# Kernel tuning notes

Measured on AMD Instinct MI355X. Metric: run time of the kernel, lower is better.

## Reference

```python
import jax, jax.numpy as jnp
import numpy as np

B, T, C = 2, 4096, 512
H = 8
D = C // H  # head_dim = 64


def setup_inputs() -> dict:
    key = jax.random.key(0)
    ks = jax.random.split(key, 9)
    s = 0.02
    return {
        "x": jax.random.normal(ks[0], (B, T, C), dtype=jnp.float32),
        "wq": jax.random.normal(ks[1], (C, C), dtype=jnp.float32) * s,
        "bq": jnp.zeros((C,), dtype=jnp.float32),
        "wk": jax.random.normal(ks[2], (C, C), dtype=jnp.float32) * s,
        "bk": jnp.zeros((C,), dtype=jnp.float32),
        "wv": jax.random.normal(ks[3], (C, C), dtype=jnp.float32) * s,
        "bv": jnp.zeros((C,), dtype=jnp.float32),
        "wo": jax.random.normal(ks[4], (C, C), dtype=jnp.float32) * s,
        "bo": jnp.zeros((C,), dtype=jnp.float32),
    }


def reference(x, wq, bq, wk, bk, wv, bv, wo, bo):
    Bx, Tx, Cx = x.shape
    # projections: y = x @ W^T + b (torch Linear convention: W is [out, in])
    q = (x @ wq.T + bq).reshape(Bx, Tx, H, D).transpose(0, 2, 1, 3)  # [B,H,T,D]
    k = (x @ wk.T + bk).reshape(Bx, Tx, H, D).transpose(0, 2, 1, 3)
    v = (x @ wv.T + bv).reshape(Bx, Tx, H, D).transpose(0, 2, 1, 3)
    scores = jnp.einsum("bhqd,bhkd->bhqk", q, k) * (D ** -0.5)  # [B,H,T,T]
    causal = jnp.tril(jnp.ones((Tx, Tx), dtype=bool))
    scores = jnp.where(causal, scores, -jnp.inf)
    weights = jax.nn.softmax(scores, axis=-1)
    o = jnp.einsum("bhqk,bhkd->bhqd", weights, v)  # [B,H,T,D]
    o = o.transpose(0, 2, 1, 3).reshape(Bx, Tx, Cx)
    return o @ wo.T + bo
```

## Files before the change

### kernel.cpp

```cpp
#include <hip/hip_runtime.h>
#include <math.h>

static constexpr int Bb = 2;
static constexpr int Tt = 4096;
static constexpr int Cc = 512;
static constexpr int Hh = 8;
static constexpr int Dd = 64;
static constexpr int Mtot = Bb * Tt;

#define QSCALE 0.1803368801111f
#define NTICK 1024

typedef __attribute__((ext_vector_type(8)))  short   short8;
typedef __attribute__((ext_vector_type(4)))  float   f32x4;
typedef __attribute__((ext_vector_type(16))) float   f32x16;
typedef __attribute__((ext_vector_type(4)))  unsigned int   uint4v;
typedef __attribute__((ext_vector_type(4)))  unsigned short ushort4v;

__device__ inline unsigned short f2bf(float f) {
    unsigned int u = __float_as_uint(f);
    u += 0x7fffu + ((u >> 16) & 1u);
    return (unsigned short)(u >> 16);
}
__device__ inline float bf2f(unsigned short u) {
    return __uint_as_float((unsigned int)u << 16);
}

__device__ inline unsigned int cvtpk_bf16(float a, float b) {
    unsigned int r;
    asm("v_cvt_pk_bf16_f32 %0, %1, %2" : "=v"(r) : "v"(a), "v"(b));
    return r;
}

__device__ inline int SW(int row) { return (row ^ (row >> 3)) & 7; }

__device__ inline void gload16(const void* g, void* lds) {
    __builtin_amdgcn_global_load_lds(
        (const __attribute__((address_space(1))) void*)g,
        (__attribute__((address_space(3))) void*)lds, 16, 0, 0);
}

__global__ __launch_bounds__(256)
void cast_f32_bf16(const float* __restrict__ src, unsigned short* __restrict__ dst,
                   int* __restrict__ ctr) {
    if (blockIdx.x == 0 && threadIdx.x == 0) *ctr = 0;
    const size_t i = ((size_t)blockIdx.x * 256 + threadIdx.x) * 8;
    const float4 a = *reinterpret_cast<const float4*>(src + i);
    const float4 b = *reinterpret_cast<const float4*>(src + i + 4);
    short8 o;
    o[0] = (short)f2bf(a.x); o[1] = (short)f2bf(a.y);
    o[2] = (short)f2bf(a.z); o[3] = (short)f2bf(a.w);
    o[4] = (short)f2bf(b.x); o[5] = (short)f2bf(b.y);
    o[6] = (short)f2bf(b.z); o[7] = (short)f2bf(b.w);
    *reinterpret_cast<short8*>(dst + i) = o;
}

__global__ __launch_bounds__(256)
void cast_w4(const float* __restrict__ w0, const float* __restrict__ w1,
             const float* __restrict__ w2, const float* __restrict__ w3,
             unsigned short* __restrict__ dst) {
    const float* srcs[4] = {w0, w1, w2, w3};
    const float* s = srcs[blockIdx.y];
    unsigned short* d = dst + (size_t)blockIdx.y * (Cc * Cc);
    const size_t i = ((size_t)blockIdx.x * 256 + threadIdx.x) * 8;
    const float4 a = *reinterpret_cast<const float4*>(s + i);
    const float4 b = *reinterpret_cast<const float4*>(s + i + 4);
    short8 o;
    o[0] = (short)f2bf(a.x); o[1] = (short)f2bf(a.y);
    o[2] = (short)f2bf(a.z); o[3] = (short)f2bf(a.w);
    o[4] = (short)f2bf(b.x); o[5] = (short)f2bf(b.y);
    o[6] = (short)f2bf(b.z); o[7] = (short)f2bf(b.w);
    *reinterpret_cast<short8*>(d + i) = o;
}

__global__ __launch_bounds__(256)
void proj_qkv(const unsigned short* __restrict__ A, const unsigned short* __restrict__ Wall,
              const float* __restrict__ bq, const float* __restrict__ bk,
              const float* __restrict__ bv,
              unsigned short* __restrict__ qo, unsigned short* __restrict__ ko,
              unsigned short* __restrict__ vo) {
    __shared__ unsigned short As[128][32];
    __shared__ unsigned short Bs[128][32];

    const int which = blockIdx.z;
    const unsigned short* Wb = Wall + (size_t)which * Cc * Cc;
    const float* bias = (which == 0) ? bq : (which == 1) ? bk : bv;
    unsigned short* outp = (which == 0) ? qo : (which == 1) ? ko : vo;
    const float scale = (which == 0) ? QSCALE : 1.0f;

    const int tid = threadIdx.x;
    const int lane = tid & 63;
    const int w = tid >> 6;
    const int wr = w >> 1, wc = w & 1;
    const int l15 = lane & 15, lg = lane >> 4;
    const int m0 = blockIdx.x * 128, n0 = blockIdx.y * 128;

    f32x4 acc[4][4] = {};

    for (int k0 = 0; k0 < Cc; k0 += 32) {
        #pragma unroll
        for (int i = 0; i < 2; ++i) {
            const int idx = tid + i * 256;
            const int row = idx >> 2, g = idx & 3;
            *reinterpret_cast<short8*>(&As[row][g * 8]) =
                *reinterpret_cast<const short8*>(&A[(size_t)(m0 + row) * Cc + k0 + g * 8]);
            *reinterpret_cast<short8*>(&Bs[row][g * 8]) =
                *reinterpret_cast<const short8*>(&Wb[(size_t)(n0 + row) * Cc + k0 + g * 8]);
        }
        __syncthreads();
        short8 a[4], b[4];
        #pragma unroll
        for (int mi = 0; mi < 4; ++mi)
            a[mi] = *reinterpret_cast<const short8*>(&As[wr * 64 + mi * 16 + l15][lg * 8]);
        #pragma unroll
        for (int nj = 0; nj < 4; ++nj)
            b[nj] = *reinterpret_cast<const short8*>(&Bs[wc * 64 + nj * 16 + l15][lg * 8]);
        #pragma unroll
        for (int mi = 0; mi < 4; ++mi)
            #pragma unroll
            for (int nj = 0; nj < 4; ++nj)
                acc[mi][nj] = __builtin_amdgcn_mfma_f32_16x16x32_bf16(a[mi], b[nj], acc[mi][nj], 0, 0, 0);
        __syncthreads();
    }

    #pragma unroll
    for (int mi = 0; mi < 4; ++mi) {
        #pragma unroll
        for (int nj = 0; nj < 4; ++nj) {
            const int col = n0 + wc * 64 + nj * 16 + l15;
            const float bvv = bias[col];
            if (which == 2) {
                const int mbase = m0 + wr * 64 + mi * 16 + lg * 4;
                const int b_ = mbase >> 12, t = mbase & (Tt - 1);
                const int h = col >> 6, d = col & 63;
                ushort4v o;
                #pragma unroll
                for (int r = 0; r < 4; ++r)
                    o[r] = f2bf(acc[mi][nj][r] + bvv);
                *reinterpret_cast<ushort4v*>(
                    &outp[(((size_t)b_ * Hh + h) * Dd + d) * Tt + t]) = o;
            } else {
                #pragma unroll
                for (int r = 0; r < 4; ++r) {
                    const int row = m0 + wr * 64 + mi * 16 + lg * 4 + r;
                    const int b_ = row >> 12, t = row & (Tt - 1);
                    const int h = col >> 6, d = col & 63;
                    outp[(((size_t)b_ * Hh + h) * Tt + t) * Dd + d] =
                        f2bf((acc[mi][nj][r] + bvv) * scale);
                }
            }
        }
    }
}

__global__ __launch_bounds__(256)
void proj_out(const unsigned short* __restrict__ A, const unsigned short* __restrict__ Wb,
              const float* __restrict__ bias, float* __restrict__ outp) {
    __shared__ unsigned short As[128][32];
    __shared__ unsigned short Bs[128][32];

    const int tid = threadIdx.x;
    const int lane = tid & 63;
    const int w = tid >> 6;
    const int wr = w >> 1, wc = w & 1;
    const int l15 = lane & 15, lg = lane >> 4;
    const int m0 = blockIdx.x * 128, n0 = blockIdx.y * 128;

    f32x4 acc[4][4] = {};

    for (int k0 = 0; k0 < Cc; k0 += 32) {
        #pragma unroll
        for (int i = 0; i < 2; ++i) {
            const int idx = tid + i * 256;
            const int row = idx >> 2, g = idx & 3;
            *reinterpret_cast<short8*>(&As[row][g * 8]) =
                *reinterpret_cast<const short8*>(&A[(size_t)(m0 + row) * Cc + k0 + g * 8]);
            *reinterpret_cast<short8*>(&Bs[row][g * 8]) =
                *reinterpret_cast<const short8*>(&Wb[(size_t)(n0 + row) * Cc + k0 + g * 8]);
        }
        __syncthreads();
        short8 a[4], b[4];
        #pragma unroll
        for (int mi = 0; mi < 4; ++mi)
            a[mi] = *reinterpret_cast<const short8*>(&As[wr * 64 + mi * 16 + l15][lg * 8]);
        #pragma unroll
        for (int nj = 0; nj < 4; ++nj)
            b[nj] = *reinterpret_cast<const short8*>(&Bs[wc * 64 + nj * 16 + l15][lg * 8]);
        #pragma unroll
        for (int mi = 0; mi < 4; ++mi)
            #pragma unroll
            for (int nj = 0; nj < 4; ++nj)
                acc[mi][nj] = __builtin_amdgcn_mfma_f32_16x16x32_bf16(a[mi], b[nj], acc[mi][nj], 0, 0, 0);
        __syncthreads();
    }

    #pragma unroll
    for (int mi = 0; mi < 4; ++mi) {
        #pragma unroll
        for (int nj = 0; nj < 4; ++nj) {
            const int col = n0 + wc * 64 + nj * 16 + l15;
            const float bv = bias[col];
            #pragma unroll
            for (int r = 0; r < 4; ++r) {
                const int row = m0 + wr * 64 + mi * 16 + lg * 4 + r;
                outp[(size_t)row * Cc + col] = acc[mi][nj][r] + bv;
            }
        }
    }
}

__global__ __launch_bounds__(512)
void attn_mfma(const unsigned short* __restrict__ qb, const unsigned short* __restrict__ kb,
               const unsigned short* __restrict__ vtb,
               unsigned short* __restrict__ opart, float* __restrict__ lp,
               int* __restrict__ ctr) {
    __shared__ unsigned short Ks[3][64][64];
    __shared__ unsigned short Vts[3][64][64];
    __shared__ int tkt;

    const int tid = threadIdx.x;
    const int w = tid >> 6;
    const int lane = tid & 63;
    const int l31 = lane & 31, hi = lane >> 5;

    const int r0 = (w << 3) + (lane >> 3);
    const int gk0 = ((lane & 7) ^ SW(r0)) * 8;

    for (;;) {
        __syncthreads();
        if (tid == 0) tkt = atomicAdd(ctr, 1);
        __syncthreads();
        const int t = tkt;
        if (t >= NTICK) break;

        const int qt = 15 - (t >> 6);
        const int ch = (t >> 4) & 3;
        const int bh = t & 15;
        const int t0 = (qt + 1) * ch;
        const int t1 = (qt + 1) * (ch + 1);

        const int qg = qt * 256 + w * 32 + l31;

        short8 qf[4];
        {
            const unsigned short* qp = qb + ((size_t)bh * Tt + qg) * Dd + hi * 8;
            #pragma unroll
            for (int sl = 0; sl < 4; ++sl)
                qf[sl] = *reinterpret_cast<const short8*>(qp + sl * 16);
        }

        const unsigned short* kb_h = kb + (size_t)bh * Tt * Dd;
        const unsigned short* vt_h = vtb + (size_t)bh * Dd * Tt;

        auto STAGE = [&](int kt_, int slot) {
            const int n64 = kt_ * 64;
            gload16(kb_h + (size_t)(n64 + r0) * Dd + gk0, &Ks[slot][(w << 3)][0]);
            gload16(vt_h + (size_t)r0 * Tt + n64 + gk0, &Vts[slot][(w << 3)][0]);
        };

        f32x16 oacc[2] = {};
        float lrow = 0.f;

        const int qmax_w = qt * 256 + w * 32 + 31;
        const int qmin_w = qt * 256 + w * 32;

        STAGE(t0, 0);
        if (t0 + 1 < t1) STAGE(t0 + 1, 1);

        int cur = 0;
        for (int kt = t0; kt < t1; ++kt) {
            if (kt + 1 < t1) {
                asm volatile("s_waitcnt vmcnt(2)" ::: "memory");
            } else {
                asm volatile("s_waitcnt vmcnt(0)" ::: "memory");
            }
            __builtin_amdgcn_s_barrier();
            __builtin_amdgcn_sched_barrier(0);

            if (kt + 2 < t1) {
                const int stg = (cur + 2 >= 3) ? (cur - 1) : (cur + 2);
                STAGE(kt + 2, stg);
            }

            if (kt * 64 <= qmax_w) {
                f32x16 sacc[2];
                __builtin_amdgcn_s_setprio(1);
                #pragma unroll
                for (int f = 0; f < 2; ++f) {
                    f32x16 z = {};
                    const int krow = f * 32 + l31;
                    const int sw = SW(krow);
                    #pragma unroll
                    for (int sl = 0; sl < 4; ++sl) {
                        const short8 kf = *reinterpret_cast<const short8*>(
                            &Ks[cur][krow][((2 * sl + hi) ^ sw) * 8]);
                        z = __builtin_amdgcn_mfma_f32_32x32x16_bf16(kf, qf[sl], z, 0, 0, 0);
                    }
                    sacc[f] = z;
                }
                __builtin_amdgcn_s_setprio(0);

                if (kt * 64 + 63 > qmin_w) {
                    #pragma unroll
                    for (int f = 0; f < 2; ++f)
                        #pragma unroll
                        for (int r = 0; r < 16; ++r) {
                            const int kvg = kt * 64 + f * 32 + (r & 3) + 8 * (r >> 2) + 4 * hi;
                            if (kvg > qg) sacc[f][r] = -INFINITY;
                        }
                }

                #pragma unroll
                for (int f = 0; f < 2; ++f)
                    #pragma unroll
                    for (int r = 0; r < 16; ++r)
                        sacc[f][r] = exp2f(sacc[f][r]);

                float t16[16];
                #pragma unroll
                for (int r = 0; r < 16; ++r) t16[r] = sacc[0][r] + sacc[1][r];
                #pragma unroll
                for (int r = 0; r < 8; ++r) t16[r] += t16[r + 8];
                #pragma unroll
                for (int r = 0; r < 4; ++r) t16[r] += t16[r + 4];
                t16[0] += t16[2];
                t16[1] += t16[3];
                lrow += t16[0] + t16[1];

                #pragma unroll
                for (int f = 0; f < 2; ++f) {
                    #pragma unroll
                    for (int s2 = 0; s2 < 2; ++s2) {
                        const int b0 = s2 * 8;
                        unsigned int c01 = cvtpk_bf16(sacc[f][b0 + 0], sacc[f][b0 + 1]);
                        unsigned int c23 = cvtpk_bf16(sacc[f][b0 + 2], sacc[f][b0 + 3]);
                        unsigned int c45 = cvtpk_bf16(sacc[f][b0 + 4], sacc[f][b0 + 5]);
                        unsigned int c67 = cvtpk_bf16(sacc[f][b0 + 6], sacc[f][b0 + 7]);
                        asm("v_permlane32_swap_b32 %0, %1" : "+v"(c01), "+v"(c45));
                        asm("v_permlane32_swap_b32 %0, %1" : "+v"(c23), "+v"(c67));
                        uint4v paw;
                        paw[0] = c01; paw[1] = c23; paw[2] = c45; paw[3] = c67;
                        const short8 pa = *reinterpret_cast<short8*>(&paw);
                        const int g = 4 * f + 2 * s2;
                        __builtin_amdgcn_s_setprio(1);
                        #pragma unroll
                        for (int nb = 0; nb < 2; ++nb) {
                            const int vrow = nb * 32 + l31;
                            const short8 vf = *reinterpret_cast<const short8*>(
                                &Vts[cur][vrow][((g + hi) ^ SW(vrow)) * 8]);
                            oacc[nb] = __builtin_amdgcn_mfma_f32_32x32x16_bf16(pa, vf, oacc[nb], 0, 0, 0);
                        }
                        __builtin_amdgcn_s_setprio(0);
                    }
                }
            }

            cur = (cur == 2) ? 0 : cur + 1;
        }

        const float lf = lrow + __shfl_xor(lrow, 32);
        const size_t pbase = ((size_t)ch * 16 + bh) * Tt;
        if (hi == 0) lp[pbase + qg] = lf;
        #pragma unroll
        for (int r = 0; r < 16; ++r) {
            const int qr = (r & 3) + 8 * (r >> 2) + 4 * hi;
            const int tg = qt * 256 + w * 32 + qr;
            unsigned short* dst = opart + (pbase + tg) * 64 + l31;
            dst[0]  = f2bf(oacc[0][r]);
            dst[32] = f2bf(oacc[1][r]);
        }
    }
}

__global__ __launch_bounds__(256)
void combine(const unsigned short* __restrict__ opart, const float* __restrict__ lp,
             unsigned short* __restrict__ ob) {
    const int tid = threadIdx.x;
    const int row = (int)blockIdx.x * 16 + (tid >> 4);
    const int c4 = (tid & 15) * 4;
    const size_t cs = (size_t)16 * Tt;

    const float inv = 1.f / (lp[row] + lp[cs + row] + lp[2 * cs + row] + lp[3 * cs + row]);

    const ushort4v p0 = *reinterpret_cast<const ushort4v*>(&opart[(0 * cs + row) * 64 + c4]);
    const ushort4v p1 = *reinterpret_cast<const ushort4v*>(&opart[(1 * cs + row) * 64 + c4]);
    const ushort4v p2 = *reinterpret_cast<const ushort4v*>(&opart[(2 * cs + row) * 64 + c4]);
    const ushort4v p3 = *reinterpret_cast<const ushort4v*>(&opart[(3 * cs + row) * 64 + c4]);

    ushort4v o;
    #pragma unroll
    for (int e = 0; e < 4; ++e)
        o[e] = f2bf((bf2f(p0[e]) + bf2f(p1[e]) + bf2f(p2[e]) + bf2f(p3[e])) * inv);

    const int bh = row >> 12, t = row & (Tt - 1);
    const int b_ = bh >> 3, h = bh & 7;
    *reinterpret_cast<ushort4v*>(&ob[((size_t)b_ * Tt + t) * Cc + h * Dd + c4]) = o;
}

extern "C" void kernel_launch(void* const* d_in, const int* in_sizes, int n_in,
                              void* d_out, int out_size, void* d_ws, size_t ws_size,
                              hipStream_t stream) {
    const float* x  = (const float*)d_in[0];
    const float* wq = (const float*)d_in[1];
    const float* bq = (const float*)d_in[2];
    const float* wk = (const float*)d_in[3];
    const float* bk = (const float*)d_in[4];
    const float* wv = (const float*)d_in[5];
    const float* bv = (const float*)d_in[6];
    const float* wo = (const float*)d_in[7];
    const float* bo = (const float*)d_in[8];
    float* out = (float*)d_out;

    const size_t nTok = (size_t)Mtot * Cc;
    const size_t nW   = (size_t)Cc * Cc;

    unsigned short* xb    = (unsigned short*)d_ws;
    unsigned short* wqb   = xb + nTok;
    unsigned short* wob   = wqb + 3 * nW;
    unsigned short* qbuf  = wqb + 4 * nW;
    unsigned short* kbuf  = qbuf + nTok;
    unsigned short* vtbuf = kbuf + nTok;
    unsigned short* oattb = vtbuf + nTok;
    unsigned short* opart = oattb + nTok;
    float* lp  = (float*)(opart + (size_t)4 * 16 * Tt * 64);
    int*   ctr = (int*)(lp + (size_t)4 * 16 * Tt);

    cast_f32_bf16<<<dim3((unsigned)(nTok / 8 / 256)), 256, 0, stream>>>(x, xb, ctr);
    cast_w4<<<dim3((unsigned)(nW / 8 / 256), 4), 256, 0, stream>>>(wq, wk, wv, wo, wqb);

    proj_qkv<<<dim3(Mtot / 128, Cc / 128, 3), 256, 0, stream>>>(
        xb, wqb, bq, bk, bv, qbuf, kbuf, vtbuf);

    attn_mfma<<<dim3(512), 512, 0, stream>>>(qbuf, kbuf, vtbuf, opart, lp, ctr);

    combine<<<dim3(16 * Tt / 16), 256, 0, stream>>>(opart, lp, oattb);

    proj_out<<<dim3(Mtot / 128, Cc / 128), 256, 0, stream>>>(oattb, wob, bo, out);
}
```

Before: 148.5 us.

## Fuse split-KV combine into output projection and merge cast kernels

The separate combine kernel is removed, and the output projection now reads the four bf16 partial attention outputs and row sums directly. It normalizes them while staging the A tile into XOR-swizzled LDS. The output GEMM tile shrinks to 64x128, the weight tile is loaded with global_load_lds, and the x and weight cast kernels are merged into a single launch. This saves two launches and the round trip of the combined attention output through memory. In exchange, each projection block redoes the combine work for every N tile, reading opart four times overall and adding more global loads to the GEMM loop.

```diff
diff --git a/kernel.cpp b/kernel.cpp
--- a/kernel.cpp
+++ b/kernel.cpp
@@ -41,10 +41,26 @@
 }
 
 __global__ __launch_bounds__(256)
-void cast_f32_bf16(const float* __restrict__ src, unsigned short* __restrict__ dst,
-                   int* __restrict__ ctr) {
-    if (blockIdx.x == 0 && threadIdx.x == 0) *ctr = 0;
-    const size_t i = ((size_t)blockIdx.x * 256 + threadIdx.x) * 8;
+void cast_all(const float* __restrict__ x,
+              const float* __restrict__ w0, const float* __restrict__ w1,
+              const float* __restrict__ w2, const float* __restrict__ w3,
+              unsigned short* __restrict__ xb, unsigned short* __restrict__ wb,
+              int* __restrict__ ctr) {
+    const int bid = (int)blockIdx.x;
+    if (bid == 0 && threadIdx.x == 0) *ctr = 0;
+    const float* src;
+    unsigned short* dst;
+    size_t i;
+    if (bid < 2048) {
+        src = x; dst = xb;
+        i = ((size_t)bid * 256 + threadIdx.x) * 8;
+    } else {
+        const float* srcs[4] = {w0, w1, w2, w3};
+        const int wi = (bid - 2048) >> 7;
+        src = srcs[wi];
+        dst = wb + (size_t)wi * (Cc * Cc);
+        i = ((size_t)((bid - 2048) & 127) * 256 + threadIdx.x) * 8;
+    }
     const float4 a = *reinterpret_cast<const float4*>(src + i);
     const float4 b = *reinterpret_cast<const float4*>(src + i + 4);
     short8 o;
@@ -56,24 +72,6 @@
 }
 
 __global__ __launch_bounds__(256)
-void cast_w4(const float* __restrict__ w0, const float* __restrict__ w1,
-             const float* __restrict__ w2, const float* __restrict__ w3,
-             unsigned short* __restrict__ dst) {
-    const float* srcs[4] = {w0, w1, w2, w3};
-    const float* s = srcs[blockIdx.y];
-    unsigned short* d = dst + (size_t)blockIdx.y * (Cc * Cc);
-    const size_t i = ((size_t)blockIdx.x * 256 + threadIdx.x) * 8;
-    const float4 a = *reinterpret_cast<const float4*>(s + i);
-    const float4 b = *reinterpret_cast<const float4*>(s + i + 4);
-    short8 o;
-    o[0] = (short)f2bf(a.x); o[1] = (short)f2bf(a.y);
-    o[2] = (short)f2bf(a.z); o[3] = (short)f2bf(a.w);
-    o[4] = (short)f2bf(b.x); o[5] = (short)f2bf(b.y);
-    o[6] = (short)f2bf(b.z); o[7] = (short)f2bf(b.w);
-    *reinterpret_cast<short8*>(d + i) = o;
-}
-
-__global__ __launch_bounds__(256)
 void proj_qkv(const unsigned short* __restrict__ A, const unsigned short* __restrict__ Wall,
               const float* __restrict__ bq, const float* __restrict__ bk,
               const float* __restrict__ bv,
@@ -154,42 +152,70 @@
 }
 
 __global__ __launch_bounds__(256)
-void proj_out(const unsigned short* __restrict__ A, const unsigned short* __restrict__ Wb,
+void proj_out(const unsigned short* __restrict__ opart, const float* __restrict__ lp,
+              const unsigned short* __restrict__ Wb,
               const float* __restrict__ bias, float* __restrict__ outp) {
-    __shared__ unsigned short As[128][32];
+    __shared__ unsigned short As[64][32];
     __shared__ unsigned short Bs[128][32];
 
     const int tid = threadIdx.x;
     const int lane = tid & 63;
     const int w = tid >> 6;
-    const int wr = w >> 1, wc = w & 1;
     const int l15 = lane & 15, lg = lane >> 4;
-    const int m0 = blockIdx.x * 128, n0 = blockIdx.y * 128;
-
-    f32x4 acc[4][4] = {};
+    const int m0 = blockIdx.x * 64, n0 = blockIdx.y * 128;
+
+    const int row_a = tid >> 2;
+    const int sg = tid & 3;
+    const int m = m0 + row_a;
+    const int b_a = m >> 12, t_a = m & (Tt - 1);
+    const size_t cs = (size_t)16 * Tt;
+
+    const int srow = (w << 4) + (lane >> 2);
+    const int sgb = lane & 3;
+
+    f32x4 acc[4][2] = {};
 
     for (int k0 = 0; k0 < Cc; k0 += 32) {
+        {
+            const int c0 = k0 + sg * 8;
+            const int h = c0 >> 6, d0 = c0 & 63;
+            const size_t rbase = ((size_t)b_a * Hh + h) * Tt + t_a;
+            const float lsum = lp[rbase] + lp[cs + rbase] +
+                               lp[2 * cs + rbase] + lp[3 * cs + rbase];
+            const float inv = 1.f / lsum;
+            float s[8] = {};
+            #pragma unroll
+            for (int chk = 0; chk < 4; ++chk) {
+                const short8 v8 = *reinterpret_cast<const short8*>(
+                    &opart[(chk * cs + rbase) * 64 + d0]);
+                #pragma unroll
+                for (int e = 0; e < 8; ++e) s[e] += bf2f((unsigned short)v8[e]);
+            }
+            short8 o8;
+            #pragma unroll
+            for (int e = 0; e < 8; ++e) o8[e] = (short)f2bf(s[e] * inv);
+            *reinterpret_cast<short8*>(&As[row_a][((sg ^ (row_a & 3))) * 8]) = o8;
+        }
         #pragma unroll
         for (int i = 0; i < 2; ++i) {
-            const int idx = tid + i * 256;
-            const int row = idx >> 2, g = idx & 3;
-            *reinterpret_cast<short8*>(&As[row][g * 8]) =
-                *reinterpret_cast<const short8*>(&A[(size_t)(m0 + row) * Cc + k0 + g * 8]);
-            *reinterpret_cast<short8*>(&Bs[row][g * 8]) =
-                *reinterpret_cast<const short8*>(&Wb[(size_t)(n0 + row) * Cc + k0 + g * 8]);
-        }
-        __syncthreads();
-        short8 a[4], b[4];
+            const int row = 64 * i + srow;
+            const int gc = (sgb ^ (row & 3)) * 8;
+            gload16(&Wb[(size_t)(n0 + row) * Cc + k0 + gc], &Bs[64 * i + (w << 4)][0]);
+        }
+        __syncthreads();
+
+        short8 a[4], b[2];
+        const int rg = (lg ^ (l15 & 3)) * 8;
         #pragma unroll
         for (int mi = 0; mi < 4; ++mi)
-            a[mi] = *reinterpret_cast<const short8*>(&As[wr * 64 + mi * 16 + l15][lg * 8]);
-        #pragma unroll
-        for (int nj = 0; nj < 4; ++nj)
-            b[nj] = *reinterpret_cast<const short8*>(&Bs[wc * 64 + nj * 16 + l15][lg * 8]);
+            a[mi] = *reinterpret_cast<const short8*>(&As[mi * 16 + l15][rg]);
+        #pragma unroll
+        for (int nj = 0; nj < 2; ++nj)
+            b[nj] = *reinterpret_cast<const short8*>(&Bs[w * 32 + nj * 16 + l15][rg]);
         #pragma unroll
         for (int mi = 0; mi < 4; ++mi)
             #pragma unroll
-            for (int nj = 0; nj < 4; ++nj)
+            for (int nj = 0; nj < 2; ++nj)
                 acc[mi][nj] = __builtin_amdgcn_mfma_f32_16x16x32_bf16(a[mi], b[nj], acc[mi][nj], 0, 0, 0);
         __syncthreads();
     }
@@ -197,12 +223,12 @@
     #pragma unroll
     for (int mi = 0; mi < 4; ++mi) {
         #pragma unroll
-        for (int nj = 0; nj < 4; ++nj) {
-            const int col = n0 + wc * 64 + nj * 16 + l15;
+        for (int nj = 0; nj < 2; ++nj) {
+            const int col = n0 + w * 32 + nj * 16 + l15;
             const float bv = bias[col];
             #pragma unroll
             for (int r = 0; r < 4; ++r) {
-                const int row = m0 + wr * 64 + mi * 16 + lg * 4 + r;
+                const int row = m0 + mi * 16 + lg * 4 + r;
                 outp[(size_t)row * Cc + col] = acc[mi][nj][r] + bv;
             }
         }
@@ -372,31 +398,6 @@
     }
 }
 
-__global__ __launch_bounds__(256)
-void combine(const unsigned short* __restrict__ opart, const float* __restrict__ lp,
-             unsigned short* __restrict__ ob) {
-    const int tid = threadIdx.x;
-    const int row = (int)blockIdx.x * 16 + (tid >> 4);
-    const int c4 = (tid & 15) * 4;
-    const size_t cs = (size_t)16 * Tt;
-
-    const float inv = 1.f / (lp[row] + lp[cs + row] + lp[2 * cs + row] + lp[3 * cs + row]);
-
-    const ushort4v p0 = *reinterpret_cast<const ushort4v*>(&opart[(0 * cs + row) * 64 + c4]);
-    const ushort4v p1 = *reinterpret_cast<const ushort4v*>(&opart[(1 * cs + row) * 64 + c4]);
-    const ushort4v p2 = *reinterpret_cast<const ushort4v*>(&opart[(2 * cs + row) * 64 + c4]);
-    const ushort4v p3 = *reinterpret_cast<const ushort4v*>(&opart[(3 * cs + row) * 64 + c4]);
-
-    ushort4v o;
-    #pragma unroll
-    for (int e = 0; e < 4; ++e)
-        o[e] = f2bf((bf2f(p0[e]) + bf2f(p1[e]) + bf2f(p2[e]) + bf2f(p3[e])) * inv);
-
-    const int bh = row >> 12, t = row & (Tt - 1);
-    const int b_ = bh >> 3, h = bh & 7;
-    *reinterpret_cast<ushort4v*>(&ob[((size_t)b_ * Tt + t) * Cc + h * Dd + c4]) = o;
-}
-
 extern "C" void kernel_launch(void* const* d_in, const int* in_sizes, int n_in,
                               void* d_out, int out_size, void* d_ws, size_t ws_size,
                               hipStream_t stream) {
@@ -420,20 +421,16 @@
     unsigned short* qbuf  = wqb + 4 * nW;
     unsigned short* kbuf  = qbuf + nTok;
     unsigned short* vtbuf = kbuf + nTok;
-    unsigned short* oattb = vtbuf + nTok;
-    unsigned short* opart = oattb + nTok;
+    unsigned short* opart = vtbuf + nTok;
     float* lp  = (float*)(opart + (size_t)4 * 16 * Tt * 64);
     int*   ctr = (int*)(lp + (size_t)4 * 16 * Tt);
 
-    cast_f32_bf16<<<dim3((unsigned)(nTok / 8 / 256)), 256, 0, stream>>>(x, xb, ctr);
-    cast_w4<<<dim3((unsigned)(nW / 8 / 256), 4), 256, 0, stream>>>(wq, wk, wv, wo, wqb);
+    cast_all<<<dim3(2560), 256, 0, stream>>>(x, wq, wk, wv, wo, xb, wqb, ctr);
 
     proj_qkv<<<dim3(Mtot / 128, Cc / 128, 3), 256, 0, stream>>>(
         xb, wqb, bq, bk, bv, qbuf, kbuf, vtbuf);
 
     attn_mfma<<<dim3(512), 512, 0, stream>>>(qbuf, kbuf, vtbuf, opart, lp, ctr);
 
-    combine<<<dim3(16 * Tt / 16), 256, 0, stream>>>(opart, lp, oattb);
-
-    proj_out<<<dim3(Mtot / 128, Cc / 128), 256, 0, stream>>>(oattb, wob, bo, out);
-}
+    proj_out<<<dim3(Mtot / 64, Cc / 128), 256, 0, stream>>>(opart, lp, wob, bo, out);
+}
```

Result: faster. 141.8 us (-4.5%).
